# Performance work log

Measured on AMD Instinct MI355X. Metric: run time of the kernel, lower is better.

## Reference

```python
import jax, jax.numpy as jnp
import numpy as np

B, H, T, K, V = 2, 8, 2048, 128, 128


def setup_inputs() -> dict:
    key = jax.random.key(0)
    k1, k2, k3, k4, k5 = jax.random.split(key, 5)
    return {
        "q": jax.random.normal(k1, (B, H, T, K), dtype=jnp.float32),
        "k": jax.random.normal(k2, (B, H, T, K), dtype=jnp.float32),
        "v": jax.random.normal(k3, (B, H, T, V), dtype=jnp.float32),
        "i_gate": jax.random.normal(k4, (B, H, T), dtype=jnp.float32),
        "f_gate": jax.random.normal(k5, (B, H, T), dtype=jnp.float32),
    }


def reference(q, k, v, i_gate, f_gate):
    # Stabilized parallel mLSTM (same math as the chunked Triton kernel,
    # expressed in natural-log base instead of base-2).
    Bq, Hq, Tq, Kd = q.shape
    scale = Kd ** -0.5
    logf = jax.nn.log_sigmoid(f_gate)                      # [B,H,T]
    fc = jnp.cumsum(logf, axis=-1)                         # cumulative forget logits
    # log decay matrix: logD[t,s] = i[s] + (fc[t] - fc[s]) for s <= t
    logD = fc[..., :, None] - fc[..., None, :] + i_gate[..., None, :]  # [B,H,T,T]
    mask = jnp.tril(jnp.ones((Tq, Tq), dtype=bool))
    logD_masked = jnp.where(mask, logD, -jnp.inf)
    m = jnp.max(logD_masked, axis=-1)                      # row-wise stabilizer [B,H,T]
    D = jnp.where(mask, jnp.exp(logD - m[..., None]), 0.0) # stabilized decay matrix
    S = jnp.einsum("bhtk,bhsk->bhts", q, k) * scale * D    # gated scores
    norm = jnp.maximum(jnp.abs(jnp.sum(S, axis=-1)), jnp.exp(-m))  # [B,H,T]
    h = jnp.einsum("bhts,bhsv->bhtv", S, v) / norm[..., None]
    return h
```

## Files before the change

### kernel.cpp

```cpp
#include <hip/hip_runtime.h>

#define T_SEQ 2048
#define DHEAD 128
#define NBH 16
#define SCALE 0.08838834764831845f

typedef unsigned short u16;
typedef u16 u16x4 __attribute__((ext_vector_type(4)));
typedef u16 u16x8 __attribute__((ext_vector_type(8)));
typedef __bf16 bf16x8 __attribute__((ext_vector_type(8)));
typedef float f32x4 __attribute__((ext_vector_type(4)));

__device__ __forceinline__ u16 f2bfu(float x) {
  union { float f; unsigned u; } c; c.f = x;
  unsigned u = c.u;
  u = u + 0x7FFFu + ((u >> 16) & 1u);
  return (u16)(u >> 16);
}

__device__ __forceinline__ bf16x8 ldsFrag(const u16* p) {
  u16x8 t = *(const u16x8*)p;
  return __builtin_bit_cast(bf16x8, t);
}

__device__ __forceinline__ void gld_lds16(const void* g, void* l) {
  __builtin_amdgcn_global_load_lds(
      (__attribute__((address_space(1))) const unsigned int*)g,
      (__attribute__((address_space(3))) unsigned int*)l, 16, 0, 0);
}

__global__ __launch_bounds__(256) void gate_scan_kernel(
    const float* __restrict__ ig, const float* __restrict__ fg,
    float* __restrict__ a_out, float* __restrict__ c_out,
    float* __restrict__ nfl_out)
{
  const int bh  = blockIdx.x;
  const int tid = threadIdx.x;
  const int base = bh * T_SEQ + tid * 8;
  __shared__ float sbuf[256];

  float lf[8];
  float run = 0.f;
#pragma unroll
  for (int j = 0; j < 8; ++j) {
    float x  = fg[base + j];
    float ls = fminf(x, 0.f) - log1pf(expf(-fabsf(x)));
    run += ls; lf[j] = run;
  }
  sbuf[tid] = run; __syncthreads();
  for (int off = 1; off < 256; off <<= 1) {
    float t = (tid >= off) ? sbuf[tid - off] : 0.f;
    __syncthreads();
    sbuf[tid] += t;
    __syncthreads();
  }
  const float excl = (tid > 0) ? sbuf[tid - 1] : 0.f;
  __syncthreads();

  float fc[8], cm[8];
  float runm = -INFINITY;
#pragma unroll
  for (int j = 0; j < 8; ++j) {
    fc[j] = excl + lf[j];
    float av = ig[base + j] - fc[j];
    a_out[base + j] = av;
    runm = fmaxf(runm, av);
    cm[j] = runm;
  }
  sbuf[tid] = runm; __syncthreads();
  for (int off = 1; off < 256; off <<= 1) {
    float t = (tid >= off) ? sbuf[tid - off] : -INFINITY;
    __syncthreads();
    sbuf[tid] = fmaxf(sbuf[tid], t);
    __syncthreads();
  }
  const float exclm = (tid > 0) ? sbuf[tid - 1] : -INFINITY;
#pragma unroll
  for (int j = 0; j < 8; ++j) {
    float c = fmaxf(exclm, cm[j]);
    c_out[base + j]   = c;
    nfl_out[base + j] = expf(-(c + fc[j]));
  }
}

__global__ __launch_bounds__(256) void cvt_k_kernel(
    const float* __restrict__ src, u16* __restrict__ dst)
{
  const int i = (blockIdx.x * 256 + threadIdx.x) * 4;
  const float4 x = *(const float4*)(src + i);
  u16x4 p; p[0] = f2bfu(x.x); p[1] = f2bfu(x.y); p[2] = f2bfu(x.z); p[3] = f2bfu(x.w);
  *(u16x4*)(dst + i) = p;
}

__global__ __launch_bounds__(256) void cvt_vt_kernel(
    const float* __restrict__ v, u16* __restrict__ vt)
{
  const int bh = blockIdx.y, kt = blockIdx.x, tid = threadIdx.x;
  __shared__ __align__(16) u16 L[128 * 72];
  const int n0 = (tid & 31) * 4, k0 = (tid >> 5) * 8;
  const float* vp = v + ((size_t)bh * T_SEQ + kt * 64 + k0) * DHEAD + n0;
  u16 tv[4][8];
#pragma unroll
  for (int rr = 0; rr < 8; ++rr) {
    const float4 x = *(const float4*)(vp + rr * DHEAD);
    tv[0][rr] = f2bfu(x.x); tv[1][rr] = f2bfu(x.y);
    tv[2][rr] = f2bfu(x.z); tv[3][rr] = f2bfu(x.w);
  }
#pragma unroll
  for (int j = 0; j < 4; ++j) {
    u16x8 p;
#pragma unroll
    for (int rr = 0; rr < 8; ++rr) p[rr] = tv[j][rr];
    *(u16x8*)(&L[(n0 + j) * 72 + k0]) = p;
  }
  __syncthreads();
  const int row = tid >> 1, s0 = (tid & 1) * 32;
  u16* op = vt + ((size_t)bh * DHEAD + row) * T_SEQ + kt * 64 + s0;
#pragma unroll
  for (int i = 0; i < 4; ++i)
    *(u16x8*)(op + i * 8) = *(const u16x8*)(&L[row * 72 + s0 + i * 8]);
}

template <bool FAST>
__global__ __launch_bounds__(512, 1) void mlstm_fwd_kernel(
    const float* __restrict__ qg, const float* __restrict__ kg,
    const float* __restrict__ vg,
    const u16* __restrict__ kbf, const u16* __restrict__ vtbf,
    const float* __restrict__ ag, const float* __restrict__ cg,
    const float* __restrict__ nflg, float* __restrict__ out)
{
  const int bx = (int)blockIdx.x;
  const int bh = bx & 15, p = bx >> 4;
  const int tid = (int)threadIdx.x;
  const int grp = tid >> 8;
  const int gt  = tid & 255;
  const int wave = gt >> 6, lane = gt & 63;
  const int quad = lane >> 4, l16 = lane & 15;
  const int w8   = tid >> 6;

  const int qt    = grp ? p : (31 - p);
  const int qtMax = 31 - p;

  __shared__ __align__(16) u16 KB[2][2][64 * 128];
  __shared__ __align__(16) u16 VB[2][2][128 * 64];
  __shared__ __align__(16) u16 Pl[8][16 * 64];

  const size_t hoff = (size_t)bh * T_SEQ * DHEAD;
  const int goff = bh * T_SEQ;
  const int qrowA = qt * 64 + wave * 16 + l16;
  const int trow0 = qt * 64 + wave * 16 + quad * 4;

  bf16x8 qf[4];
  {
    const float* qp = qg + hoff + (size_t)qrowA * DHEAD + quad * 8;
#pragma unroll
    for (int kc = 0; kc < 4; ++kc) {
      const float4 x0 = *(const float4*)(qp + kc * 32);
      const float4 x1 = *(const float4*)(qp + kc * 32 + 4);
      u16x8 t;
      t[0] = f2bfu(x0.x); t[1] = f2bfu(x0.y); t[2] = f2bfu(x0.z); t[3] = f2bfu(x0.w);
      t[4] = f2bfu(x1.x); t[5] = f2bfu(x1.y); t[6] = f2bfu(x1.z); t[7] = f2bfu(x1.w);
      qf[kc] = __builtin_bit_cast(bf16x8, t);
    }
  }
  const float cmax = cg[goff + qt * 64 + 63];

  f32x4 oa[8];
#pragma unroll
  for (int nv = 0; nv < 8; ++nv) oa[nv] = (f32x4){0.f, 0.f, 0.f, 0.f};
  float rs[4] = {0.f, 0.f, 0.f, 0.f};

  float4 kr[8], vr[8];
  const int fb_keyb = gt >> 4;
  const int fb_db   = (gt & 15) ^ ((gt >> 4) & 7);
  const int fb_n0 = (gt & 31) * 4, fb_k0 = (gt >> 5) * 8;

  auto stage_issue = [&](int kt, int b) {
    if (FAST) {
      const u16* ks = kbf + ((size_t)goff + kt * 64) * DHEAD;
      const u16* vs = vtbf + (size_t)bh * DHEAD * T_SEQ + kt * 64;
#pragma unroll
      for (int j = 0; j < 4; ++j) {
        const int B = (wave * 4 + j) * 64 + lane;
        {
          const int key = B >> 4;
          const int db = (B & 15) ^ (key & 7);
          gld_lds16(ks + (size_t)key * DHEAD + db * 8, &KB[grp][b][(wave * 4 + j) * 512]);
        }
        {
          const int n = B >> 3;
          const int kb = (B & 7) ^ (n & 7);
          gld_lds16(vs + (size_t)n * T_SEQ + kb * 8, &VB[grp][b][(wave * 4 + j) * 512]);
        }
      }
    } else {
      const float* kp = kg + hoff + (size_t)(kt * 64) * DHEAD;
      const float* vp = vg + hoff + (size_t)(kt * 64 + fb_k0) * DHEAD + fb_n0;
#pragma unroll
      for (int jb = 0; jb < 4; ++jb) {
        const int key = fb_keyb + 16 * jb;
        kr[2 * jb]     = *(const float4*)(kp + (size_t)key * DHEAD + fb_db * 8);
        kr[2 * jb + 1] = *(const float4*)(kp + (size_t)key * DHEAD + fb_db * 8 + 4);
      }
#pragma unroll
      for (int rr = 0; rr < 8; ++rr) vr[rr] = *(const float4*)(vp + rr * DHEAD);
    }
  };
  auto stage_commit = [&](int b) {
    if (!FAST) {
#pragma unroll
      for (int jb = 0; jb < 4; ++jb) {
        const int key = fb_keyb + 16 * jb;
        u16x8 pk;
        pk[0] = f2bfu(kr[2*jb].x);   pk[1] = f2bfu(kr[2*jb].y);
        pk[2] = f2bfu(kr[2*jb].z);   pk[3] = f2bfu(kr[2*jb].w);
        pk[4] = f2bfu(kr[2*jb+1].x); pk[5] = f2bfu(kr[2*jb+1].y);
        pk[6] = f2bfu(kr[2*jb+1].z); pk[7] = f2bfu(kr[2*jb+1].w);
        *(u16x8*)(&KB[grp][b][(key * 16 + (gt & 15)) * 8]) = pk;
      }
      u16 tv[4][8];
#pragma unroll
      for (int rr = 0; rr < 8; ++rr) {
        tv[0][rr] = f2bfu(vr[rr].x); tv[1][rr] = f2bfu(vr[rr].y);
        tv[2][rr] = f2bfu(vr[rr].z); tv[3][rr] = f2bfu(vr[rr].w);
      }
      const int kb = fb_k0 >> 3;
#pragma unroll
      for (int j = 0; j < 4; ++j) {
        const int n = fb_n0 + j;
        u16x8 pk;
#pragma unroll
        for (int rr = 0; rr < 8; ++rr) pk[rr] = tv[j][rr];
        *(u16x8*)(&VB[grp][b][(n * 8 + (kb ^ (n & 7))) * 8]) = pk;
      }
    }
  };

  stage_issue(0, 0);
  stage_commit(0);
  __syncthreads();

  for (int kt = 0; kt <= qtMax; ++kt) {
    const int b = kt & 1;
    const bool act = (kt <= qt);
    if (act && kt < qt) stage_issue(kt + 1, b ^ 1);

    if (act) {
      float an[4];
#pragma unroll
      for (int nc = 0; nc < 4; ++nc) an[nc] = ag[goff + kt * 64 + nc * 16 + l16];

      const bool diag = (kt == qt);
#pragma unroll
      for (int nc = 0; nc < 4; ++nc) {
        f32x4 s = (f32x4){0.f, 0.f, 0.f, 0.f};
        const int key = nc * 16 + l16;
#pragma unroll
        for (int kc = 0; kc < 4; ++kc) {
          const int db = (kc * 4 + quad) ^ (l16 & 7);
          const bf16x8 bk = ldsFrag(&KB[grp][b][(key * 16 + db) * 8]);
          s = __builtin_amdgcn_mfma_f32_16x16x32_bf16(qf[kc], bk, s, 0, 0, 0);
        }
        const float es = SCALE * __expf(an[nc] - cmax);
        const int scol = nc * 16 + l16;
#pragma unroll
        for (int r = 0; r < 4; ++r) {
          float pv = s[r] * es;
          if (diag && (kt * 64 + scol > trow0 + r)) pv = 0.f;
          rs[r] += pv;
          const int m = quad * 4 + r;
          Pl[w8][m * 64 + ((((scol >> 3) ^ (m & 7)) << 3) | (scol & 7))] = f2bfu(pv);
        }
      }
#pragma unroll
      for (int kk = 0; kk < 2; ++kk) {
        const bf16x8 pa = ldsFrag(&Pl[w8][l16 * 64 + (((kk * 4 + quad) ^ (l16 & 7)) << 3)]);
#pragma unroll
        for (int nv = 0; nv < 8; ++nv) {
          const int n = nv * 16 + l16;
          const int kb = (kk * 4 + quad) ^ (l16 & 7);
          const bf16x8 bv = ldsFrag(&VB[grp][b][(n * 8 + kb) * 8]);
          oa[nv] = __builtin_amdgcn_mfma_f32_16x16x32_bf16(pa, bv, oa[nv], 0, 0, 0);
        }
      }
    }
    if (act && kt < qt) stage_commit(b ^ 1);
    __syncthreads();
  }

#pragma unroll
  for (int r = 0; r < 4; ++r) {
    float x = rs[r];
#pragma unroll
    for (int off = 1; off < 16; off <<= 1) x += __shfl_xor(x, off, 64);
    rs[r] = x;
  }
  float inv[4];
#pragma unroll
  for (int r = 0; r < 4; ++r) {
    const float crv  = cg[goff + trow0 + r];
    const float erow = __expf(cmax - crv);
    const float nf   = nflg[goff + trow0 + r];
    inv[r] = erow / fmaxf(fabsf(rs[r] * erow), nf);
  }
  float* op = out + hoff;
#pragma unroll
  for (int nv = 0; nv < 8; ++nv) {
#pragma unroll
    for (int r = 0; r < 4; ++r) {
      op[(size_t)(trow0 + r) * DHEAD + nv * 16 + l16] = oa[nv][r] * inv[r];
    }
  }
}

extern "C" void kernel_launch(void* const* d_in, const int* in_sizes, int n_in,
                              void* d_out, int out_size, void* d_ws, size_t ws_size,
                              hipStream_t stream) {
  const float* q  = (const float*)d_in[0];
  const float* k  = (const float*)d_in[1];
  const float* v  = (const float*)d_in[2];
  const float* ig = (const float*)d_in[3];
  const float* fg = (const float*)d_in[4];

  const size_t gate_bytes = (size_t)3 * NBH * T_SEQ * sizeof(float);
  const size_t kv_elems   = (size_t)NBH * T_SEQ * DHEAD;
  const bool fast = ws_size >= gate_bytes + 2 * kv_elems * sizeof(u16);

  float* a_ws   = (float*)d_ws;
  float* c_ws   = a_ws + NBH * T_SEQ;
  float* nfl_ws = c_ws + NBH * T_SEQ;
  u16* kbf  = (u16*)((char*)d_ws + gate_bytes);
  u16* vtbf = kbf + kv_elems;

  gate_scan_kernel<<<dim3(NBH), dim3(256), 0, stream>>>(ig, fg, a_ws, c_ws, nfl_ws);
  if (fast) {
    cvt_k_kernel<<<dim3((unsigned)(kv_elems / 1024)), dim3(256), 0, stream>>>(k, kbf);
    cvt_vt_kernel<<<dim3(T_SEQ / 64, NBH), dim3(256), 0, stream>>>(v, vtbf);
    mlstm_fwd_kernel<true><<<dim3(256), dim3(512), 0, stream>>>(
        q, k, v, kbf, vtbf, a_ws, c_ws, nfl_ws, (float*)d_out);
  } else {
    mlstm_fwd_kernel<false><<<dim3(256), dim3(512), 0, stream>>>(
        q, k, v, kbf, vtbf, a_ws, c_ws, nfl_ws, (float*)d_out);
  }
}
```

Baseline: 158.0 us.

## Switch to 32x32x16 MFMA with shared K/V tiles and key-split waves

```diff
diff --git a/kernel.cpp b/kernel.cpp
--- a/kernel.cpp
+++ b/kernel.cpp
@@ -9,7 +9,7 @@
 typedef u16 u16x4 __attribute__((ext_vector_type(4)));
 typedef u16 u16x8 __attribute__((ext_vector_type(8)));
 typedef __bf16 bf16x8 __attribute__((ext_vector_type(8)));
-typedef float f32x4 __attribute__((ext_vector_type(4)));
+typedef float f32x16 __attribute__((ext_vector_type(16)));
 
 __device__ __forceinline__ u16 f2bfu(float x) {
   union { float f; unsigned u; } c; c.f = x;
@@ -32,7 +32,7 @@
 __global__ __launch_bounds__(256) void gate_scan_kernel(
     const float* __restrict__ ig, const float* __restrict__ fg,
     float* __restrict__ a_out, float* __restrict__ c_out,
-    float* __restrict__ nfl_out)
+    float* __restrict__ fc_out)
 {
   const int bh  = blockIdx.x;
   const int tid = threadIdx.x;
@@ -62,6 +62,7 @@
 #pragma unroll
   for (int j = 0; j < 8; ++j) {
     fc[j] = excl + lf[j];
+    fc_out[base + j] = fc[j];
     float av = ig[base + j] - fc[j];
     a_out[base + j] = av;
     runm = fmaxf(runm, av);
@@ -77,9 +78,7 @@
   const float exclm = (tid > 0) ? sbuf[tid - 1] : -INFINITY;
 #pragma unroll
   for (int j = 0; j < 8; ++j) {
-    float c = fmaxf(exclm, cm[j]);
-    c_out[base + j]   = c;
-    nfl_out[base + j] = expf(-(c + fc[j]));
+    c_out[base + j] = fmaxf(exclm, cm[j]);
   }
 }
 
@@ -122,116 +121,108 @@
 }
 
 template <bool FAST>
-__global__ __launch_bounds__(512, 1) void mlstm_fwd_kernel(
+__global__ __launch_bounds__(512, 2) void mlstm_fwd_kernel(
     const float* __restrict__ qg, const float* __restrict__ kg,
     const float* __restrict__ vg,
     const u16* __restrict__ kbf, const u16* __restrict__ vtbf,
     const float* __restrict__ ag, const float* __restrict__ cg,
-    const float* __restrict__ nflg, float* __restrict__ out)
+    const float* __restrict__ fcg, float* __restrict__ out)
 {
   const int bx = (int)blockIdx.x;
   const int bh = bx & 15, p = bx >> 4;
   const int tid = (int)threadIdx.x;
-  const int grp = tid >> 8;
-  const int gt  = tid & 255;
-  const int wave = gt >> 6, lane = gt & 63;
-  const int quad = lane >> 4, l16 = lane & 15;
-  const int w8   = tid >> 6;
-
-  const int qt    = grp ? p : (31 - p);
-  const int qtMax = 31 - p;
-
-  __shared__ __align__(16) u16 KB[2][2][64 * 128];
-  __shared__ __align__(16) u16 VB[2][2][128 * 64];
-  __shared__ __align__(16) u16 Pl[8][16 * 64];
+  const int w8 = tid >> 6, lane = tid & 63;
+  const int hh = lane >> 5, l32 = lane & 31;
+
+  const int qsel  = w8 >> 2;
+  const int half  = (w8 >> 1) & 1;
+  const int strip = w8 & 1;
+  const int qt    = qsel ? p : (31 - p);
+  const int nST   = 32 - p;
+  const int diagST = qsel ? p : (31 - p);
+  const int qrow0 = qt * 64 + strip * 32;
+
+  __shared__ __align__(16) unsigned char SM[81920];
+  u16* Plw = (u16*)(SM + 65536 + w8 * 2048);
 
   const size_t hoff = (size_t)bh * T_SEQ * DHEAD;
   const int goff = bh * T_SEQ;
-  const int qrowA = qt * 64 + wave * 16 + l16;
-  const int trow0 = qt * 64 + wave * 16 + quad * 4;
-
-  bf16x8 qf[4];
+
+  bf16x8 qf[8];
   {
-    const float* qp = qg + hoff + (size_t)qrowA * DHEAD + quad * 8;
-#pragma unroll
-    for (int kc = 0; kc < 4; ++kc) {
-      const float4 x0 = *(const float4*)(qp + kc * 32);
-      const float4 x1 = *(const float4*)(qp + kc * 32 + 4);
+    const float* qp = qg + hoff + (size_t)(qrow0 + l32) * DHEAD + hh * 8;
+#pragma unroll
+    for (int ks_ = 0; ks_ < 8; ++ks_) {
+      const float4 x0 = *(const float4*)(qp + ks_ * 16);
+      const float4 x1 = *(const float4*)(qp + ks_ * 16 + 4);
       u16x8 t;
       t[0] = f2bfu(x0.x); t[1] = f2bfu(x0.y); t[2] = f2bfu(x0.z); t[3] = f2bfu(x0.w);
       t[4] = f2bfu(x1.x); t[5] = f2bfu(x1.y); t[6] = f2bfu(x1.z); t[7] = f2bfu(x1.w);
-      qf[kc] = __builtin_bit_cast(bf16x8, t);
+      qf[ks_] = __builtin_bit_cast(bf16x8, t);
     }
   }
   const float cmax = cg[goff + qt * 64 + 63];
 
-  f32x4 oa[8];
-#pragma unroll
-  for (int nv = 0; nv < 8; ++nv) oa[nv] = (f32x4){0.f, 0.f, 0.f, 0.f};
-  float rs[4] = {0.f, 0.f, 0.f, 0.f};
-
-  float4 kr[8], vr[8];
-  const int fb_keyb = gt >> 4;
-  const int fb_db   = (gt & 15) ^ ((gt >> 4) & 7);
-  const int fb_n0 = (gt & 31) * 4, fb_k0 = (gt >> 5) * 8;
-
-  auto stage_issue = [&](int kt, int b) {
+  f32x16 oa[4];
+#pragma unroll
+  for (int nt = 0; nt < 4; ++nt)
+#pragma unroll
+    for (int r = 0; r < 16; ++r) oa[nt][r] = 0.f;
+  float rs[16];
+#pragma unroll
+  for (int r = 0; r < 16; ++r) rs[r] = 0.f;
+
+  float kr[2][8], vr[2][8];
+
+  auto stage_issue = [&](int st, int b) {
     if (FAST) {
-      const u16* ks = kbf + ((size_t)goff + kt * 64) * DHEAD;
-      const u16* vs = vtbf + (size_t)bh * DHEAD * T_SEQ + kt * 64;
-#pragma unroll
-      for (int j = 0; j < 4; ++j) {
-        const int B = (wave * 4 + j) * 64 + lane;
+      const u16* ks = kbf + ((size_t)goff + st * 64) * DHEAD;
+      const u16* vs = vtbf + (size_t)bh * DHEAD * T_SEQ + st * 64;
+#pragma unroll
+      for (int j = 0; j < 2; ++j) {
+        const int B = (w8 * 2 + j) * 64 + lane;
         {
           const int key = B >> 4;
           const int db = (B & 15) ^ (key & 7);
-          gld_lds16(ks + (size_t)key * DHEAD + db * 8, &KB[grp][b][(wave * 4 + j) * 512]);
+          gld_lds16(ks + (size_t)key * DHEAD + db * 8,
+                    (u16*)(SM + b * 32768) + (w8 * 2 + j) * 512);
         }
         {
           const int n = B >> 3;
           const int kb = (B & 7) ^ (n & 7);
-          gld_lds16(vs + (size_t)n * T_SEQ + kb * 8, &VB[grp][b][(wave * 4 + j) * 512]);
+          gld_lds16(vs + (size_t)n * T_SEQ + kb * 8,
+                    (u16*)(SM + b * 32768 + 16384) + (w8 * 2 + j) * 512);
         }
       }
     } else {
-      const float* kp = kg + hoff + (size_t)(kt * 64) * DHEAD;
-      const float* vp = vg + hoff + (size_t)(kt * 64 + fb_k0) * DHEAD + fb_n0;
-#pragma unroll
-      for (int jb = 0; jb < 4; ++jb) {
-        const int key = fb_keyb + 16 * jb;
-        kr[2 * jb]     = *(const float4*)(kp + (size_t)key * DHEAD + fb_db * 8);
-        kr[2 * jb + 1] = *(const float4*)(kp + (size_t)key * DHEAD + fb_db * 8 + 4);
-      }
-#pragma unroll
-      for (int rr = 0; rr < 8; ++rr) vr[rr] = *(const float4*)(vp + rr * DHEAD);
+      const float* kp = kg + hoff + (size_t)(st * 64) * DHEAD;
+      const float* vp = vg + hoff + (size_t)(st * 64) * DHEAD;
+#pragma unroll
+      for (int j = 0; j < 2; ++j) {
+        const int B = (w8 * 2 + j) * 64 + lane;
+        const int key = B >> 4;
+        const int db = (B & 15) ^ (key & 7);
+        const float4 x0 = *(const float4*)(kp + (size_t)key * DHEAD + db * 8);
+        const float4 x1 = *(const float4*)(kp + (size_t)key * DHEAD + db * 8 + 4);
+        kr[j][0] = x0.x; kr[j][1] = x0.y; kr[j][2] = x0.z; kr[j][3] = x0.w;
+        kr[j][4] = x1.x; kr[j][5] = x1.y; kr[j][6] = x1.z; kr[j][7] = x1.w;
+        const int n = B >> 3;
+        const int kb = (B & 7) ^ (n & 7);
+#pragma unroll
+        for (int rr = 0; rr < 8; ++rr)
+          vr[j][rr] = vp[(size_t)(kb * 8 + rr) * DHEAD + n];
+      }
     }
   };
   auto stage_commit = [&](int b) {
     if (!FAST) {
 #pragma unroll
-      for (int jb = 0; jb < 4; ++jb) {
-        const int key = fb_keyb + 16 * jb;
-        u16x8 pk;
-        pk[0] = f2bfu(kr[2*jb].x);   pk[1] = f2bfu(kr[2*jb].y);
-        pk[2] = f2bfu(kr[2*jb].z);   pk[3] = f2bfu(kr[2*jb].w);
-        pk[4] = f2bfu(kr[2*jb+1].x); pk[5] = f2bfu(kr[2*jb+1].y);
-        pk[6] = f2bfu(kr[2*jb+1].z); pk[7] = f2bfu(kr[2*jb+1].w);
-        *(u16x8*)(&KB[grp][b][(key * 16 + (gt & 15)) * 8]) = pk;
-      }
-      u16 tv[4][8];
-#pragma unroll
-      for (int rr = 0; rr < 8; ++rr) {
-        tv[0][rr] = f2bfu(vr[rr].x); tv[1][rr] = f2bfu(vr[rr].y);
-        tv[2][rr] = f2bfu(vr[rr].z); tv[3][rr] = f2bfu(vr[rr].w);
-      }
-      const int kb = fb_k0 >> 3;
-#pragma unroll
-      for (int j = 0; j < 4; ++j) {
-        const int n = fb_n0 + j;
-        u16x8 pk;
-#pragma unroll
-        for (int rr = 0; rr < 8; ++rr) pk[rr] = tv[j][rr];
-        *(u16x8*)(&VB[grp][b][(n * 8 + (kb ^ (n & 7))) * 8]) = pk;
+      for (int j = 0; j < 2; ++j) {
+        u16x8 pk, pv;
+#pragma unroll
+        for (int rr = 0; rr < 8; ++rr) { pk[rr] = f2bfu(kr[j][rr]); pv[rr] = f2bfu(vr[j][rr]); }
+        *(u16x8*)((u16*)(SM + b * 32768) + (w8 * 2 + j) * 512 + lane * 8) = pk;
+        *(u16x8*)((u16*)(SM + b * 32768 + 16384) + (w8 * 2 + j) * 512 + lane * 8) = pv;
       }
     }
   };
@@ -240,76 +231,103 @@
   stage_commit(0);
   __syncthreads();
 
-  for (int kt = 0; kt <= qtMax; ++kt) {
-    const int b = kt & 1;
-    const bool act = (kt <= qt);
-    if (act && kt < qt) stage_issue(kt + 1, b ^ 1);
-
+  const int plc = (lane >> 3) & 3, pl7 = lane & 7;
+
+  for (int st = 0; st < nST; ++st) {
+    const int b = st & 1;
+    if (st + 1 < nST) stage_issue(st + 1, b ^ 1);
+
+    const bool act = (qsel == 0) || (st <= p);
     if (act) {
-      float an[4];
-#pragma unroll
-      for (int nc = 0; nc < 4; ++nc) an[nc] = ag[goff + kt * 64 + nc * 16 + l16];
-
-      const bool diag = (kt == qt);
-#pragma unroll
-      for (int nc = 0; nc < 4; ++nc) {
-        f32x4 s = (f32x4){0.f, 0.f, 0.f, 0.f};
-        const int key = nc * 16 + l16;
-#pragma unroll
-        for (int kc = 0; kc < 4; ++kc) {
-          const int db = (kc * 4 + quad) ^ (l16 & 7);
-          const bf16x8 bk = ldsFrag(&KB[grp][b][(key * 16 + db) * 8]);
-          s = __builtin_amdgcn_mfma_f32_16x16x32_bf16(qf[kc], bk, s, 0, 0, 0);
+      const int keyl = half * 32 + l32;
+      const int keyg = st * 64 + keyl;
+      const float av = ag[goff + keyg];
+      const u16* Kb_ = (const u16*)(SM + b * 32768);
+      const u16* Vb_ = (const u16*)(SM + b * 32768 + 16384);
+
+      f32x16 s;
+#pragma unroll
+      for (int r = 0; r < 16; ++r) s[r] = 0.f;
+#pragma unroll
+      for (int ks_ = 0; ks_ < 8; ++ks_) {
+        const int db = 2 * ks_ + hh;
+        const bf16x8 bk = ldsFrag(Kb_ + keyl * 128 + ((db ^ (keyl & 7)) * 8));
+        s = __builtin_amdgcn_mfma_f32_32x32x16_bf16(qf[ks_], bk, s, 0, 0, 0);
+      }
+      const float es = SCALE * __expf(av - cmax);
+      const bool diag = (st == diagST);
+#pragma unroll
+      for (int reg = 0; reg < 16; ++reg) {
+        const int rowl = (reg & 3) + 8 * (reg >> 2) + 4 * hh;
+        float pv = s[reg] * es;
+        if (diag && (keyg > qrow0 + rowl)) pv = 0.f;
+        rs[reg] += pv;
+        Plw[rowl * 32 + ((plc ^ (rowl & 3)) * 8) + pl7] = f2bfu(pv);
+      }
+#pragma unroll
+      for (int k2 = 0; k2 < 2; ++k2) {
+        const int cb = 2 * k2 + hh;
+        const bf16x8 pa = ldsFrag(Plw + l32 * 32 + ((cb ^ (l32 & 3)) * 8));
+        const int kb = half * 4 + 2 * k2 + hh;
+#pragma unroll
+        for (int nt = 0; nt < 4; ++nt) {
+          const int n = nt * 32 + l32;
+          const bf16x8 bv = ldsFrag(Vb_ + n * 64 + ((kb ^ (n & 7)) * 8));
+          oa[nt] = __builtin_amdgcn_mfma_f32_32x32x16_bf16(pa, bv, oa[nt], 0, 0, 0);
         }
-        const float es = SCALE * __expf(an[nc] - cmax);
-        const int scol = nc * 16 + l16;
-#pragma unroll
-        for (int r = 0; r < 4; ++r) {
-          float pv = s[r] * es;
-          if (diag && (kt * 64 + scol > trow0 + r)) pv = 0.f;
-          rs[r] += pv;
-          const int m = quad * 4 + r;
-          Pl[w8][m * 64 + ((((scol >> 3) ^ (m & 7)) << 3) | (scol & 7))] = f2bfu(pv);
-        }
-      }
-#pragma unroll
-      for (int kk = 0; kk < 2; ++kk) {
-        const bf16x8 pa = ldsFrag(&Pl[w8][l16 * 64 + (((kk * 4 + quad) ^ (l16 & 7)) << 3)]);
-#pragma unroll
-        for (int nv = 0; nv < 8; ++nv) {
-          const int n = nv * 16 + l16;
-          const int kb = (kk * 4 + quad) ^ (l16 & 7);
-          const bf16x8 bv = ldsFrag(&VB[grp][b][(n * 8 + kb) * 8]);
-          oa[nv] = __builtin_amdgcn_mfma_f32_16x16x32_bf16(pa, bv, oa[nv], 0, 0, 0);
-        }
-      }
-    }
-    if (act && kt < qt) stage_commit(b ^ 1);
-    __syncthreads();
-  }
-
-#pragma unroll
-  for (int r = 0; r < 4; ++r) {
-    float x = rs[r];
-#pragma unroll
-    for (int off = 1; off < 16; off <<= 1) x += __shfl_xor(x, off, 64);
-    rs[r] = x;
-  }
-  float inv[4];
-#pragma unroll
-  for (int r = 0; r < 4; ++r) {
-    const float crv  = cg[goff + trow0 + r];
-    const float erow = __expf(cmax - crv);
-    const float nf   = nflg[goff + trow0 + r];
-    inv[r] = erow / fmaxf(fabsf(rs[r] * erow), nf);
-  }
-  float* op = out + hoff;
-#pragma unroll
-  for (int nv = 0; nv < 8; ++nv) {
-#pragma unroll
-    for (int r = 0; r < 4; ++r) {
-      op[(size_t)(trow0 + r) * DHEAD + nv * 16 + l16] = oa[nv][r] * inv[r];
-    }
+      }
+    }
+    if (st + 1 < nST) stage_commit(b ^ 1);
+    __syncthreads();
+  }
+
+  float* osh = (float*)SM;
+  float* rsh = (float*)(SM + 65536);
+  const int combo = qsel * 2 + strip;
+
+#pragma unroll
+  for (int reg = 0; reg < 16; ++reg) {
+    float x = rs[reg];
+#pragma unroll
+    for (int off = 1; off < 32; off <<= 1) x += __shfl_xor(x, off, 64);
+    rs[reg] = x;
+  }
+
+  if (half == 1) {
+#pragma unroll
+    for (int nt = 0; nt < 4; ++nt)
+#pragma unroll
+      for (int reg = 0; reg < 16; ++reg) {
+        const int rowl = (reg & 3) + 8 * (reg >> 2) + 4 * hh;
+        osh[combo * 4096 + rowl * 128 + nt * 32 + l32] = oa[nt][reg];
+      }
+    if (l32 == 0) {
+#pragma unroll
+      for (int reg = 0; reg < 16; ++reg) {
+        const int rowl = (reg & 3) + 8 * (reg >> 2) + 4 * hh;
+        rsh[combo * 32 + rowl] = rs[reg];
+      }
+    }
+  }
+  __syncthreads();
+  if (half == 0) {
+    float inv[16];
+#pragma unroll
+    for (int reg = 0; reg < 16; ++reg) {
+      const int rowl = (reg & 3) + 8 * (reg >> 2) + 4 * hh;
+      const float rtot = rs[reg] + rsh[combo * 32 + rowl];
+      const float fcv = fcg[goff + qrow0 + rowl];
+      inv[reg] = 1.f / fmaxf(fabsf(rtot), __expf(-(cmax + fcv)));
+    }
+    float* op = out + hoff;
+#pragma unroll
+    for (int nt = 0; nt < 4; ++nt)
+#pragma unroll
+      for (int reg = 0; reg < 16; ++reg) {
+        const int rowl = (reg & 3) + 8 * (reg >> 2) + 4 * hh;
+        const float ov = oa[nt][reg] + osh[combo * 4096 + rowl * 128 + nt * 32 + l32];
+        op[(size_t)(qrow0 + rowl) * DHEAD + nt * 32 + l32] = ov * inv[reg];
+      }
   }
 }
 
@@ -326,20 +344,20 @@
   const size_t kv_elems   = (size_t)NBH * T_SEQ * DHEAD;
   const bool fast = ws_size >= gate_bytes + 2 * kv_elems * sizeof(u16);
 
-  float* a_ws   = (float*)d_ws;
-  float* c_ws   = a_ws + NBH * T_SEQ;
-  float* nfl_ws = c_ws + NBH * T_SEQ;
+  float* a_ws  = (float*)d_ws;
+  float* c_ws  = a_ws + NBH * T_SEQ;
+  float* fc_ws = c_ws + NBH * T_SEQ;
   u16* kbf  = (u16*)((char*)d_ws + gate_bytes);
   u16* vtbf = kbf + kv_elems;
 
-  gate_scan_kernel<<<dim3(NBH), dim3(256), 0, stream>>>(ig, fg, a_ws, c_ws, nfl_ws);
+  gate_scan_kernel<<<dim3(NBH), dim3(256), 0, stream>>>(ig, fg, a_ws, c_ws, fc_ws);
   if (fast) {
     cvt_k_kernel<<<dim3((unsigned)(kv_elems / 1024)), dim3(256), 0, stream>>>(k, kbf);
     cvt_vt_kernel<<<dim3(T_SEQ / 64, NBH), dim3(256), 0, stream>>>(v, vtbf);
     mlstm_fwd_kernel<true><<<dim3(256), dim3(512), 0, stream>>>(
-        q, k, v, kbf, vtbf, a_ws, c_ws, nfl_ws, (float*)d_out);
+        q, k, v, kbf, vtbf, a_ws, c_ws, fc_ws, (float*)d_out);
   } else {
     mlstm_fwd_kernel<false><<<dim3(256), dim3(512), 0, stream>>>(
-        q, k, v, kbf, vtbf, a_ws, c_ws, nfl_ws, (float*)d_out);
-  }
-}
+        q, k, v, kbf, vtbf, a_ws, c_ws, fc_ws, (float*)d_out);
+  }
+}
```

New measurement: 150.7 us. -4.6%, faster.
